# Performance work log

Hardware: AMD Instinct MI355X
Metric: run time of the kernel (lower is better)

Reference implementation:

```python
import jax, jax.numpy as jnp
import numpy as np

VOCAB = 50000
EMB = 64
HID = 64


def _lstm_final(emb_t, mask_t, W, U, b):
    # emb_t: (T, B, EMB), mask_t: (T, B) bool. Keras gate order: i, f, g(c), o.
    B = emb_t.shape[1]
    h0 = jnp.zeros((B, HID), emb_t.dtype)
    c0 = jnp.zeros((B, HID), emb_t.dtype)

    def step(carry, xm):
        h, c = carry
        x, m = xm
        z = x @ W + h @ U + b  # (B, 4H)
        i, f, g, o = jnp.split(z, 4, axis=-1)
        i = jax.nn.sigmoid(i)
        f = jax.nn.sigmoid(f)
        g = jnp.tanh(g)
        o = jax.nn.sigmoid(o)
        c_new = f * c + i * g
        h_new = o * jnp.tanh(c_new)
        m = m[:, None]
        h = jnp.where(m, h_new, h)  # masked steps carry state through
        c = jnp.where(m, c_new, c)
        return (h, c), None

    (h, c), _ = jax.lax.scan(step, (h0, c0), (emb_t, mask_t))
    return h


def setup_inputs() -> dict:
    key = jax.random.key(0)
    ks = jax.random.split(key, 12)
    B, T = 512, 1024
    x = jax.random.randint(ks[0], (B, T), 0, VOCAB + 1, dtype=jnp.int64)
    s = 0.05
    inp = {
        "x": x,
        "emb_table": jax.random.normal(ks[1], (VOCAB + 1, EMB), jnp.float32) * s,
        "Wf": jax.random.normal(ks[2], (EMB, 4 * HID), jnp.float32) * s,
        "Uf": jax.random.normal(ks[3], (HID, 4 * HID), jnp.float32) * s,
        "bf": jnp.zeros((4 * HID,), jnp.float32),
        "Wb": jax.random.normal(ks[4], (EMB, 4 * HID), jnp.float32) * s,
        "Ub": jax.random.normal(ks[5], (HID, 4 * HID), jnp.float32) * s,
        "bb": jnp.zeros((4 * HID,), jnp.float32),
        "W1": jax.random.normal(ks[6], (2 * HID, 32), jnp.float32) * s,
        "b1": jnp.zeros((32,), jnp.float32),
        "W2": jax.random.normal(ks[7], (32, 1), jnp.float32) * s,
        "b2": jnp.zeros((1,), jnp.float32),
    }
    return inp


def reference(x, emb_table, Wf, Uf, bf, Wb, Ub, bb, W1, b1, W2, b2):
    mask = x != 0  # (B, T) mask_zero
    emb = emb_table[x]  # (B, T, EMB)
    emb_t = jnp.transpose(emb, (1, 0, 2))  # (T, B, EMB)
    mask_t = jnp.transpose(mask, (1, 0))   # (T, B)
    h_fwd = _lstm_final(emb_t, mask_t, Wf, Uf, bf)
    h_bwd = _lstm_final(emb_t[::-1], mask_t[::-1], Wb, Ub, bb)
    h = jnp.concatenate([h_fwd, h_bwd], axis=-1)  # (B, 2H)
    h = jax.nn.relu(h @ W1 + b1)  # dropout is identity at inference
    out = h @ W2 + b2  # (B, 1)
    return out
```

## Files before the change

### kernel.cpp

```cpp
#include <hip/hip_runtime.h>

#define T 1024
#define BATCH 512
#define EMB 64
#define HID 64
#define NGATE 256
#define VOCABP1 50001

typedef unsigned int uint32;
typedef unsigned short u16;
typedef __attribute__((ext_vector_type(8))) short short8;
typedef __attribute__((ext_vector_type(4))) float f32x4;
typedef __attribute__((ext_vector_type(4))) float float4v;

#define L2E 1.44269504088896340736f

__device__ __forceinline__ float rcpf(float x) { return __builtin_amdgcn_rcpf(x); }
__device__ __forceinline__ float exp2as(float x) {
    float r;
    asm("v_exp_f32 %0, %1" : "=v"(r) : "v"(x));
    return r;
}
__device__ __forceinline__ float sigm_pre(float z)  { return rcpf(1.0f + exp2as(z)); }
__device__ __forceinline__ float tanh_pre(float z)  { return fmaf(-2.0f, rcpf(exp2as(z) + 1.0f), 1.0f); }
__device__ __forceinline__ float tanh_c(float c)    { return tanh_pre(c * (2.0f * L2E)); }

__device__ __forceinline__ u16 f2bf(float x) {
    uint32 u = __float_as_uint(x);
    u += 0x7fffu + ((u >> 16) & 1u);
    return (u16)(u >> 16);
}
__device__ __forceinline__ float bf2f(u16 h) { return __uint_as_float(((uint32)h) << 16); }

#define BARRIER_LDS() asm volatile("s_waitcnt lgkmcnt(0)\n\ts_barrier" ::: "memory")

__global__ void prep_kernel(const int* __restrict__ x, const float* __restrict__ emb,
                            const float* __restrict__ Uf, const float* __restrict__ Ub,
                            const float* __restrict__ Wf, const float* __restrict__ Wb,
                            u16* __restrict__ xstream, uint32* __restrict__ mbits,
                            u16* __restrict__ bfrag)
{
    const int bid = blockIdx.x;
    const int tid = threadIdx.x;

    if (bid < 2048) {
        const int gb    = bid >> 6;
        const int stile = bid & 63;
        const int lane  = tid & 63;
        const int half  = tid >> 6;
        const int ks    = half & 1;
        const int sp    = half >> 1;
        const int m     = lane & 15;
        const int qj    = (lane >> 4) * 8;
#pragma unroll
        for (int i = 0; i < 8; ++i) {
            const int s   = stile * 16 + sp * 8 + i;
            const int tok = x[(gb * 16 + m) * T + s];
            const float* er = emb + (size_t)tok * EMB + ks * 32 + qj;
            const float4v a = *(const float4v*)er;
            const float4v b = *(const float4v*)(er + 4);
            short8 v;
            v[0] = (short)f2bf(a[0]); v[1] = (short)f2bf(a[1]);
            v[2] = (short)f2bf(a[2]); v[3] = (short)f2bf(a[3]);
            v[4] = (short)f2bf(b[0]); v[5] = (short)f2bf(b[1]);
            v[6] = (short)f2bf(b[2]); v[7] = (short)f2bf(b[3]);
            *(short8*)(xstream + ((size_t)(gb * 1024 + s) * 128 + ks * 64 + lane) * 8) = v;
        }
    } else if (bid < 2048 + 128) {
        const int idx  = (bid - 2048) * 256 + tid;
        const int word = idx & 31;
        const int db   = idx >> 5;
        const int d    = db >> 9;
        const int b    = db & 511;
        const int* src = x + b * T;
        uint32 m = 0;
#pragma unroll 8
        for (int i = 0; i < 32; ++i) {
            const int t = word * 32 + i;
            m |= (src[d ? (T - 1 - t) : t] != 0 ? 1u : 0u) << i;
        }
        mbits[idx] = m;
    } else {
        const int bid3 = bid - 2176;
        const int d  = bid3 >> 3;
        const int g  = (bid3 >> 1) & 3;
        const int ks = bid3 & 1;
        const float* U = d ? Ub : Uf;
        const float* W = d ? Wb : Wf;
        const int lane = tid & 63, w = tid >> 6;
        const float scale = (g == 2) ? (2.0f * L2E) : (-L2E);
#pragma unroll
        for (int j = 0; j < 8; ++j) {
            const int col = g * 64 + 16 * w + (lane & 15);
            const int k   = ks * 32 + (lane >> 4) * 8 + j;
            const float uv = U[k * NGATE + col] * scale;
            const u16 uhi = f2bf(uv);
            const u16 ulo = f2bf(uv - bf2f(uhi));
            const u16 whi = f2bf(W[k * NGATE + col] * scale);
            const size_t base = ((((size_t)(d * 4 + w) * 4 + g) * 2 + ks) * 3) * 512;
            bfrag[base + 0 * 512 + lane * 8 + j] = uhi;
            bfrag[base + 1 * 512 + lane * 8 + j] = ulo;
            bfrag[base + 2 * 512 + lane * 8 + j] = whi;
        }
    }
}

__global__ __launch_bounds__(256, 1)
void lstm_mfma(const uint32* __restrict__ mbits,
               const u16* __restrict__ xstream,
               const u16* __restrict__ bfragp,
               const float* __restrict__ bf, const float* __restrict__ bb,
               float* __restrict__ hcat)
{
    const int tid  = threadIdx.x;
    const int lane = tid & 63;
    const int w    = tid >> 6;
    const int col  = lane & 15;
    const int quad = lane >> 4;
    const int gb16  = blockIdx.x & 31;
    const int inner = blockIdx.x >> 5;
    const int d     = inner >> 2;
    const int sub   = inner & 3;

    const int ucol = 16 * w + col;
    const int KS   = w >> 1;

    short8 BUh[4][2];
    short8 BW[4][2];
    {
        const u16* pb = bfragp + (size_t)(d * 4 + w) * 4 * 2 * 3 * 512;
#pragma unroll
        for (int g = 0; g < 4; ++g)
#pragma unroll
        for (int ks = 0; ks < 2; ++ks) {
            BUh[g][ks] = *(const short8*)&pb[((g * 2 + ks) * 3 + 0) * 512 + lane * 8];
            BW[g][ks]  = *(const short8*)&pb[((g * 2 + ks) * 3 + 2) * 512 + lane * 8];
        }
    }
    float biasv[4];
    {
        const float* bias = d ? bb : bf;
#pragma unroll
        for (int g = 0; g < 4; ++g)
            biasv[g] = bias[g * 64 + ucol] * ((g == 2) ? (2.0f * L2E) : (-L2E));
    }

    __shared__ u16 Ahl[2][2][64][8];
    {
        u16* f = &Ahl[0][0][0][0];
        for (int i = tid; i < 2 * 2 * 64 * 8; i += 256) f[i] = 0;
    }

    const uint32* mrow = mbits + (size_t)(d * 512 + gb16 * 16 + 4 * sub + quad) * 32;
    uint32 mcur = mrow[0], mnext = mrow[1];
    const int q2u  = (2 * w + (col >> 3)) & 3;
    const int hrow = q2u * 16 + 4 * quad;
    const int hj   = col & 7;

    const u16* sptr = xstream + (size_t)gb16 * 1024 * 1024;

    const int srcoff    = ((lane & 48) | (4 * sub + ((lane & 15) >> 2))) * 8;
    const int lanedelta = srcoff + (d ? -(lane & 3) : (lane & 3)) * 1024;

#define XBATCH(XT, G)                                                          \
    XT[G][0] = biasv[G]; XT[G][1] = biasv[G];                                  \
    XT[G][2] = biasv[G]; XT[G][3] = biasv[G];                                  \
    XT[G] = __builtin_amdgcn_mfma_f32_16x16x32_bf16(axr[0], BW[G][0], XT[G], 0, 0, 0); \
    XT[G] = __builtin_amdgcn_mfma_f32_16x16x32_bf16(axr[1], BW[G][1], XT[G], 0, 0, 0);

    short8 axr[2];
    f32x4  xaccA[4], xaccB[4];
    {
        const int c2 = d ? 1023 : 0;
        const u16* cp = sptr + (size_t)c2 * 1024;
        axr[0] = *(const short8*)(cp + lanedelta);
        axr[1] = *(const short8*)(cp + 512 + lanedelta);
        XBATCH(xaccA, 0) XBATCH(xaccA, 1) XBATCH(xaccA, 2) XBATCH(xaccA, 3)
    }
    f32x4 xinit[4];
#pragma unroll
    for (int g = 0; g < 4; ++g) { xinit[g][0] = 0.f; xinit[g][1] = 0.f; xinit[g][2] = 0.f; xinit[g][3] = 0.f; }

    __syncthreads();

    float hv = 0.f, cv = 0.f;

#define STEP(SV, P, XC, XP, QP)                                                \
  {                                                                            \
    if ((QP) == 0) {        \
      const int cs = ((SV) + 4 <= 1020) ? ((SV) + 4) : 1020;                   \
      const int c2 = d ? (1023 - cs) : cs;                                     \
      const u16* cp = sptr + (size_t)c2 * 1024;                                \
      axr[0] = *(const short8*)(cp + lanedelta);                               \
      axr[1] = *(const short8*)(cp + 512 + lanedelta);                         \
      if ((((SV) & 31) == 0) && ((SV) > 0)) {                                  \
        const int wn = ((SV) >> 5) + 1;                                        \
        const int wc = (wn < 32) ? wn : 31;                                    \
        mcur = mnext; mnext = mrow[wc];                                        \
      }                                                                        \
    }                                                                          \
    BARRIER_LDS();                                                             \
    const short8 Ah0 = *(const short8*)&Ahl[1 - (P)][0][lane][0];              \
    const short8 Ah1 = *(const short8*)&Ahl[1 - (P)][1][lane][0];              \
                  \
    xinit[0][0] = XC[0][(QP)];                                                 \
    xinit[1][0] = XC[1][(QP)];                                                 \
    xinit[2][0] = XC[2][(QP)];                                                 \
    xinit[3][0] = XC[3][(QP)];                                                 \
    if ((QP) == 2) { XBATCH(XP, 0) XBATCH(XP, 1) }                             \
    if ((QP) == 3) { XBATCH(XP, 2) XBATCH(XP, 3) }                             \
    \
    f32x4 a2 = __builtin_amdgcn_mfma_f32_16x16x32_bf16(Ah0, BUh[2][0], xinit[2], 0, 0, 0); \
    a2       = __builtin_amdgcn_mfma_f32_16x16x32_bf16(Ah1, BUh[2][1], a2, 0, 0, 0);       \
    f32x4 a0 = __builtin_amdgcn_mfma_f32_16x16x32_bf16(Ah0, BUh[0][0], xinit[0], 0, 0, 0); \
    a0       = __builtin_amdgcn_mfma_f32_16x16x32_bf16(Ah1, BUh[0][1], a0, 0, 0, 0);       \
    f32x4 a1 = __builtin_amdgcn_mfma_f32_16x16x32_bf16(Ah0, BUh[1][0], xinit[1], 0, 0, 0); \
    a1       = __builtin_amdgcn_mfma_f32_16x16x32_bf16(Ah1, BUh[1][1], a1, 0, 0, 0);       \
    f32x4 a3 = __builtin_amdgcn_mfma_f32_16x16x32_bf16(Ah0, BUh[3][0], xinit[3], 0, 0, 0); \
    a3       = __builtin_amdgcn_mfma_f32_16x16x32_bf16(Ah1, BUh[3][1], a3, 0, 0, 0);       \
         \
    {                                                                          \
      const float gg = a2[0] + a2[1];                                          \
      const float gv = tanh_pre(gg);                                           \
      const float gi = a0[0] + a0[1];                                          \
      const float iv = sigm_pre(gi);                                           \
      const float gf = a1[0] + a1[1];                                          \
      const float fv = sigm_pre(gf);                                           \
      const float ig = iv * gv;                                                \
      const float cn = fmaf(fv, cv, ig);                                       \
      const float go = a3[0] + a3[1];                                          \
      const float ov = sigm_pre(go);                                           \
      const float th = tanh_c(cn);                                             \
      const float hn = ov * th;                                                \
      if ((mcur >> ((SV) & 31)) & 1) { cv = cn; hv = hn; }                     \
      const uint32 uh = __float_as_uint(hv);                                   \
      const u16 hhi = (u16)(uh >> 16);                                         \
      const u16 hlo = (u16)(__float_as_uint(hv - bf2f(hhi)) >> 16);            \
      Ahl[(P)][KS][hrow][hj]     = hhi;                                        \
      Ahl[(P)][KS][hrow + 1][hj] = hlo;                                        \
    }                                                                          \
  }

    for (int s = 0; s < T; s += 8) {
        STEP(s,     0, xaccA, xaccB, 0)
        STEP(s + 1, 1, xaccA, xaccB, 1)
        STEP(s + 2, 0, xaccA, xaccB, 2)
        STEP(s + 3, 1, xaccA, xaccB, 3)
        STEP(s + 4, 0, xaccB, xaccA, 0)
        STEP(s + 5, 1, xaccB, xaccA, 1)
        STEP(s + 6, 0, xaccB, xaccA, 2)
        STEP(s + 7, 1, xaccB, xaccA, 3)
    }
#undef STEP
#undef XBATCH

    hcat[(size_t)(gb16 * 16 + 4 * sub + quad) * (2 * HID) + d * HID + ucol] = hv;
}

__global__ void mlp_kernel(const float* __restrict__ hcat,
                           const float* __restrict__ W1, const float* __restrict__ b1,
                           const float* __restrict__ W2, const float* __restrict__ b2,
                           float* __restrict__ out)
{
    const int b = blockIdx.x;
    const int tid = threadIdx.x;
    __shared__ float h1[32];
    const float* h = hcat + b * (2 * HID);
    if (tid < 32) {
        float acc = b1[tid];
#pragma unroll
        for (int k = 0; k < 2 * HID; ++k) acc += h[k] * W1[k * 32 + tid];
        h1[tid] = fmaxf(acc, 0.0f);
    }
    __syncthreads();
    if (tid == 0) {
        float acc = b2[0];
#pragma unroll
        for (int m = 0; m < 32; ++m) acc += h1[m] * W2[m];
        out[b] = acc;
    }
}

extern "C" void kernel_launch(void* const* d_in, const int* in_sizes, int n_in,
                              void* d_out, int out_size, void* d_ws, size_t ws_size,
                              hipStream_t stream)
{
    const int*   x   = (const int*)d_in[0];
    const float* emb = (const float*)d_in[1];
    const float* Wf  = (const float*)d_in[2];
    const float* Uf  = (const float*)d_in[3];
    const float* bf  = (const float*)d_in[4];
    const float* Wb  = (const float*)d_in[5];
    const float* Ub  = (const float*)d_in[6];
    const float* bb  = (const float*)d_in[7];
    const float* W1  = (const float*)d_in[8];
    const float* b1  = (const float*)d_in[9];
    const float* W2  = (const float*)d_in[10];
    const float* b2  = (const float*)d_in[11];
    float* out = (float*)d_out;

    u16*    xstream = (u16*)d_ws;
    uint32* mbits   = (uint32*)(xstream + (size_t)32 * 1024 * 1024);
    u16*    bfragp  = (u16*)(mbits + 2 * 512 * 32);
    float*  hcat    = (float*)(bfragp + 98304);

    prep_kernel<<<dim3(2048 + 128 + 16), dim3(256), 0, stream>>>(
        x, emb, Uf, Ub, Wf, Wb, xstream, mbits, bfragp);
    lstm_mfma<<<dim3(256), dim3(256), 0, stream>>>(mbits, xstream, bfragp, bf, bb, hcat);
    mlp_kernel<<<dim3(BATCH), dim3(64), 0, stream>>>(hcat, W1, b1, W2, b2, out);
}
```

Before: 379.6 us.

## Fuse embedding gather into LSTM kernel, drop bf16 xstream prepass

Removes the prep stage that gathered embeddings, converted them to bf16 and wrote a 64 MB staging stream. The LSTM kernel now reads token ids itself, prefetching them two groups ahead, gathers the fp32 embedding rows directly, and packs them to bf16 with v_cvt_pk_bf16_f32 before the input MFMAs. This avoids the extra write and read of the staged stream and a large kernel launch. In exchange it puts dependent gather latency (token, then row) and wider fp32 loads inside the serial recurrence loop.

```diff
diff --git a/kernel.cpp b/kernel.cpp
--- a/kernel.cpp
+++ b/kernel.cpp
@@ -12,6 +12,7 @@
 typedef __attribute__((ext_vector_type(8))) short short8;
 typedef __attribute__((ext_vector_type(4))) float f32x4;
 typedef __attribute__((ext_vector_type(4))) float float4v;
+typedef __attribute__((ext_vector_type(4))) uint32 u32x4;
 
 #define L2E 1.44269504088896340736f
 
@@ -32,42 +33,24 @@
 }
 __device__ __forceinline__ float bf2f(u16 h) { return __uint_as_float(((uint32)h) << 16); }
 
+__device__ __forceinline__ uint32 cvtpk(float a, float b) {
+    uint32 r;
+    asm("v_cvt_pk_bf16_f32 %0, %1, %2" : "=v"(r) : "v"(a), "v"(b));
+    return r;
+}
+
 #define BARRIER_LDS() asm volatile("s_waitcnt lgkmcnt(0)\n\ts_barrier" ::: "memory")
 
-__global__ void prep_kernel(const int* __restrict__ x, const float* __restrict__ emb,
+__global__ void prep_kernel(const int* __restrict__ x,
                             const float* __restrict__ Uf, const float* __restrict__ Ub,
                             const float* __restrict__ Wf, const float* __restrict__ Wb,
-                            u16* __restrict__ xstream, uint32* __restrict__ mbits,
-                            u16* __restrict__ bfrag)
+                            uint32* __restrict__ mbits, u16* __restrict__ bfrag)
 {
     const int bid = blockIdx.x;
     const int tid = threadIdx.x;
 
-    if (bid < 2048) {
-        const int gb    = bid >> 6;
-        const int stile = bid & 63;
-        const int lane  = tid & 63;
-        const int half  = tid >> 6;
-        const int ks    = half & 1;
-        const int sp    = half >> 1;
-        const int m     = lane & 15;
-        const int qj    = (lane >> 4) * 8;
-#pragma unroll
-        for (int i = 0; i < 8; ++i) {
-            const int s   = stile * 16 + sp * 8 + i;
-            const int tok = x[(gb * 16 + m) * T + s];
-            const float* er = emb + (size_t)tok * EMB + ks * 32 + qj;
-            const float4v a = *(const float4v*)er;
-            const float4v b = *(const float4v*)(er + 4);
-            short8 v;
-            v[0] = (short)f2bf(a[0]); v[1] = (short)f2bf(a[1]);
-            v[2] = (short)f2bf(a[2]); v[3] = (short)f2bf(a[3]);
-            v[4] = (short)f2bf(b[0]); v[5] = (short)f2bf(b[1]);
-            v[6] = (short)f2bf(b[2]); v[7] = (short)f2bf(b[3]);
-            *(short8*)(xstream + ((size_t)(gb * 1024 + s) * 128 + ks * 64 + lane) * 8) = v;
-        }
-    } else if (bid < 2048 + 128) {
-        const int idx  = (bid - 2048) * 256 + tid;
+    if (bid < 128) {
+        const int idx  = bid * 256 + tid;
         const int word = idx & 31;
         const int db   = idx >> 5;
         const int d    = db >> 9;
@@ -81,7 +64,7 @@
         }
         mbits[idx] = m;
     } else {
-        const int bid3 = bid - 2176;
+        const int bid3 = bid - 128;
         const int d  = bid3 >> 3;
         const int g  = (bid3 >> 1) & 3;
         const int ks = bid3 & 1;
@@ -107,7 +90,8 @@
 
 __global__ __launch_bounds__(256, 1)
 void lstm_mfma(const uint32* __restrict__ mbits,
-               const u16* __restrict__ xstream,
+               const int* __restrict__ x,
+               const float* __restrict__ emb,
                const u16* __restrict__ bfragp,
                const float* __restrict__ bf, const float* __restrict__ bb,
                float* __restrict__ hcat)
@@ -157,10 +141,10 @@
     const int hrow = q2u * 16 + 4 * quad;
     const int hj   = col & 7;
 
-    const u16* sptr = xstream + (size_t)gb16 * 1024 * 1024;
-
-    const int srcoff    = ((lane & 48) | (4 * sub + ((lane & 15) >> 2))) * 8;
-    const int lanedelta = srcoff + (d ? -(lane & 3) : (lane & 3)) * 1024;
+    const int seqg  = gb16 * 16 + 4 * sub + ((lane & 15) >> 2);
+    const int xbase = seqg * T;
+    const int qj8   = (lane >> 4) * 8;
+    const int lofs  = lane & 3;
 
 #define XBATCH(XT, G)                                                          \
     XT[G][0] = biasv[G]; XT[G][1] = biasv[G];                                  \
@@ -168,14 +152,33 @@
     XT[G] = __builtin_amdgcn_mfma_f32_16x16x32_bf16(axr[0], BW[G][0], XT[G], 0, 0, 0); \
     XT[G] = __builtin_amdgcn_mfma_f32_16x16x32_bf16(axr[1], BW[G][1], XT[G], 0, 0, 0);
 
+#define CVT_AXR()                                                              \
+    {                                                                          \
+      u32x4 t0, t1;                                                            \
+      t0[0] = cvtpk(e0[0], e0[1]); t0[1] = cvtpk(e0[2], e0[3]);                \
+      t0[2] = cvtpk(e1[0], e1[1]); t0[3] = cvtpk(e1[2], e1[3]);                \
+      t1[0] = cvtpk(e2[0], e2[1]); t1[1] = cvtpk(e2[2], e2[3]);                \
+      t1[2] = cvtpk(e3[0], e3[1]); t1[3] = cvtpk(e3[2], e3[3]);                \
+      axr[0] = *(short8*)&t0;                                                  \
+      axr[1] = *(short8*)&t1;                                                  \
+    }
+
     short8 axr[2];
     f32x4  xaccA[4], xaccB[4];
+    float4v e0, e1, e2, e3;
+    int tokA, tokB;
     {
-        const int c2 = d ? 1023 : 0;
-        const u16* cp = sptr + (size_t)c2 * 1024;
-        axr[0] = *(const short8*)(cp + lanedelta);
-        axr[1] = *(const short8*)(cp + 512 + lanedelta);
+        const int st0 = lofs;
+        const int tok0 = x[xbase + (d ? (1023 - st0) : st0)];
+        const float* er = emb + (size_t)tok0 * EMB + qj8;
+        e0 = *(const float4v*)er;
+        e1 = *(const float4v*)(er + 4);
+        e2 = *(const float4v*)(er + 32);
+        e3 = *(const float4v*)(er + 36);
+        CVT_AXR()
         XBATCH(xaccA, 0) XBATCH(xaccA, 1) XBATCH(xaccA, 2) XBATCH(xaccA, 3)
+        const int st4 = 4 + lofs;
+        tokA = x[xbase + (d ? (1023 - st4) : st4)];
     }
     f32x4 xinit[4];
 #pragma unroll
@@ -185,14 +188,17 @@
 
     float hv = 0.f, cv = 0.f;
 
-#define STEP(SV, P, XC, XP, QP)                                                \
+#define STEP(SV, P, XC, XP, QP, TC, TN)                                        \
   {                                                                            \
-    if ((QP) == 0) {        \
-      const int cs = ((SV) + 4 <= 1020) ? ((SV) + 4) : 1020;                   \
-      const int c2 = d ? (1023 - cs) : cs;                                     \
-      const u16* cp = sptr + (size_t)c2 * 1024;                                \
-      axr[0] = *(const short8*)(cp + lanedelta);                               \
-      axr[1] = *(const short8*)(cp + 512 + lanedelta);                         \
+    if ((QP) == 0) {      \
+      const float* er = emb + (size_t)(TC) * EMB + qj8;                        \
+      e0 = *(const float4v*)er;                                                \
+      e1 = *(const float4v*)(er + 4);                                          \
+      e2 = *(const float4v*)(er + 32);                                         \
+      e3 = *(const float4v*)(er + 36);                                         \
+      const int cs2 = ((SV) + 8 <= 1020) ? ((SV) + 8) : 1020;                  \
+      const int st2 = cs2 + lofs;                                              \
+      TN = x[xbase + (d ? (1023 - st2) : st2)];                                \
       if ((((SV) & 31) == 0) && ((SV) > 0)) {                                  \
         const int wn = ((SV) >> 5) + 1;                                        \
         const int wc = (wn < 32) ? wn : 31;                                    \
@@ -202,12 +208,12 @@
     BARRIER_LDS();                                                             \
     const short8 Ah0 = *(const short8*)&Ahl[1 - (P)][0][lane][0];              \
     const short8 Ah1 = *(const short8*)&Ahl[1 - (P)][1][lane][0];              \
-                  \
+            \
     xinit[0][0] = XC[0][(QP)];                                                 \
     xinit[1][0] = XC[1][(QP)];                                                 \
     xinit[2][0] = XC[2][(QP)];                                                 \
     xinit[3][0] = XC[3][(QP)];                                                 \
-    if ((QP) == 2) { XBATCH(XP, 0) XBATCH(XP, 1) }                             \
+    if ((QP) == 2) { CVT_AXR() XBATCH(XP, 0) XBATCH(XP, 1) }                   \
     if ((QP) == 3) { XBATCH(XP, 2) XBATCH(XP, 3) }                             \
     \
     f32x4 a2 = __builtin_amdgcn_mfma_f32_16x16x32_bf16(Ah0, BUh[2][0], xinit[2], 0, 0, 0); \
@@ -242,17 +248,18 @@
   }
 
     for (int s = 0; s < T; s += 8) {
-        STEP(s,     0, xaccA, xaccB, 0)
-        STEP(s + 1, 1, xaccA, xaccB, 1)
-        STEP(s + 2, 0, xaccA, xaccB, 2)
-        STEP(s + 3, 1, xaccA, xaccB, 3)
-        STEP(s + 4, 0, xaccB, xaccA, 0)
-        STEP(s + 5, 1, xaccB, xaccA, 1)
-        STEP(s + 6, 0, xaccB, xaccA, 2)
-        STEP(s + 7, 1, xaccB, xaccA, 3)
+        STEP(s,     0, xaccA, xaccB, 0, tokA, tokB)
+        STEP(s + 1, 1, xaccA, xaccB, 1, tokA, tokB)
+        STEP(s + 2, 0, xaccA, xaccB, 2, tokA, tokB)
+        STEP(s + 3, 1, xaccA, xaccB, 3, tokA, tokB)
+        STEP(s + 4, 0, xaccB, xaccA, 0, tokB, tokA)
+        STEP(s + 5, 1, xaccB, xaccA, 1, tokB, tokA)
+        STEP(s + 6, 0, xaccB, xaccA, 2, tokB, tokA)
+        STEP(s + 7, 1, xaccB, xaccA, 3, tokB, tokA)
     }
 #undef STEP
 #undef XBATCH
+#undef CVT_AXR
 
     hcat[(size_t)(gb16 * 16 + 4 * sub + quad) * (2 * HID) + d * HID + ucol] = hv;
 }
@@ -304,8 +311,8 @@
     u16*    bfragp  = (u16*)(mbits + 2 * 512 * 32);
     float*  hcat    = (float*)(bfragp + 98304);
 
-    prep_kernel<<<dim3(2048 + 128 + 16), dim3(256), 0, stream>>>(
-        x, emb, Uf, Ub, Wf, Wb, xstream, mbits, bfragp);
-    lstm_mfma<<<dim3(256), dim3(256), 0, stream>>>(mbits, xstream, bfragp, bf, bb, hcat);
+    prep_kernel<<<dim3(128 + 16), dim3(256), 0, stream>>>(
+        x, Uf, Ub, Wf, Wb, mbits, bfragp);
+    lstm_mfma<<<dim3(256), dim3(256), 0, stream>>>(mbits, x, emb, bfragp, bf, bb, hcat);
     mlp_kernel<<<dim3(BATCH), dim3(64), 0, stream>>>(hcat, W1, b1, W2, b2, out);
 }
```

Measured after the change: 487.5 us. 28.4% more time.
